# Optimization experiments

Hardware: AMD Instinct MI355X
Metric: run time of the kernel (lower is better)

The kernel has to match this reference:

```python
import jax, jax.numpy as jnp
import numpy as np

EPS = 1e-5
N_HEADS = 8
NEG = -1e32


def _pos_emb(S, D):
    # CosinePositionalEmbedding: sin/cos fully overwrite the random init for even D
    pos = jnp.arange(S, dtype=jnp.float32)[:, None]
    div = jnp.exp(jnp.arange(0, D, 2, dtype=jnp.float32) * (-np.log(10000.0) / D))
    pe = jnp.zeros((S, D), dtype=jnp.float32)
    pe = pe.at[:, 0::2].set(jnp.sin(pos * div))
    pe = pe.at[:, 1::2].set(jnp.cos(pos * div))
    return pe


def _ln(x, g, b):
    mu = jnp.mean(x, axis=-1, keepdims=True)
    var = jnp.mean((x - mu) ** 2, axis=-1, keepdims=True)
    return (x - mu) / jnp.sqrt(var + EPS) * g + b


def setup_inputs() -> dict:
    key = jax.random.key(0)
    B, S, D, FF, L = 32, 512, 512, 2048, 4
    ks = jax.random.split(key, 8)
    w = 0.02
    return {
        "q_embed_data": jax.random.normal(ks[0], (B, S, D), jnp.float32),
        "qa_embed_data": jax.random.normal(ks[1], (B, S, D), jnp.float32),
        "boost_focus": jax.random.uniform(ks[2], (1,), jnp.float32),
        "Wk": w * jax.random.normal(ks[3], (L, D, D), jnp.float32),
        "bk": jnp.zeros((L, D), jnp.float32),
        "Wv": w * jax.random.normal(ks[4], (L, D, D), jnp.float32),
        "bv": jnp.zeros((L, D), jnp.float32),
        "Wo": w * jax.random.normal(ks[5], (L, D, D), jnp.float32),
        "bo": jnp.zeros((L, D), jnp.float32),
        "ln1_g": jnp.ones((L, D), jnp.float32),
        "ln1_b": jnp.zeros((L, D), jnp.float32),
        "W1": w * jax.random.normal(ks[6], (L, D, FF), jnp.float32),
        "b1": jnp.zeros((L, FF), jnp.float32),
        "W2": w * jax.random.normal(ks[7], (L, FF, D), jnp.float32),
        "b2": jnp.zeros((L, D), jnp.float32),
        "ln2_g": jnp.ones((L, D), jnp.float32),
        "ln2_b": jnp.zeros((L, D), jnp.float32),
    }


def reference(q_embed_data, qa_embed_data, boost_focus, Wk, bk, Wv, bv, Wo, bo,
              ln1_g, ln1_b, W1, b1, W2, b2, ln2_g, ln2_b):
    B, S, D = q_embed_data.shape
    L = Wk.shape[0]
    H = N_HEADS
    dk = D // H
    bf = boost_focus[0]
    pe = _pos_emb(S, D)
    x = q_embed_data + pe[None]          # query/key stream
    y = qa_embed_data + pe[None]         # value stream (fixed across blocks)
    # mask=0: triu(k=0)==0 -> only strictly past positions (j < i) allowed
    allowed = jnp.tril(jnp.ones((S, S), bool), k=-1)
    scale = 1.0 / np.sqrt(dk)
    for l in range(L):
        # kq_same=True: q and k both use k_linear on x -> identical projections
        qk = (x @ Wk[l] + bk[l]).reshape(B, S, H, dk).transpose(0, 2, 1, 3)
        v = (y @ Wv[l] + bv[l]).reshape(B, S, H, dk).transpose(0, 2, 1, 3)
        scores = jnp.einsum('bhid,bhjd->bhij', qk, qk) * scale * (1.0 + bf)
        scores = jnp.where(allowed, scores, NEG)
        probs = jax.nn.softmax(scores, axis=-1)
        probs = probs.at[:, :, 0, :].set(0.0)  # zero_pad: first query row zeroed
        attn = jnp.einsum('bhij,bhjd->bhid', probs, v)
        attn = attn.transpose(0, 2, 1, 3).reshape(B, S, D) @ Wo[l] + bo[l]
        x = _ln(x + attn, ln1_g[l], ln1_b[l])
        ff = jax.nn.relu(x @ W1[l] + b1[l]) @ W2[l] + b2[l]
        x = _ln(x + ff, ln2_g[l], ln2_b[l])
    return x
```

## Files before the change

kernel.cpp:

```cpp
#include <hip/hip_runtime.h>
#include <hip/hip_bf16.h>

typedef __bf16 bf16_t;
typedef __bf16 bf16x4 __attribute__((ext_vector_type(4)));
typedef __bf16 bf16x8 __attribute__((ext_vector_type(8)));
typedef float f32x4 __attribute__((ext_vector_type(4)));

union FragU { bf16x8 v; bf16x4 h[2]; };
union F4U { float4 v; float f[4]; };

constexpr int BB = 32, SS = 512, DD = 512, FFD = 2048, LL = 4, HH = 8;

__device__ __forceinline__ int permk(int k) {
  int g = (k >> 2) & 7;
  int pos = (g < 4) ? (g << 1) : (((g - 4) << 1) | 1);
  return (k & ~31) | (pos << 2) | (k & 3);
}

__device__ __forceinline__ void gload_lds16(const bf16_t* g, bf16_t* l) {
  __builtin_amdgcn_global_load_lds(
      (const __attribute__((address_space(1))) void*)g,
      (__attribute__((address_space(3))) void*)l, 16, 0, 0);
}

template<int N> __device__ __forceinline__ void vmwait() {
  asm volatile("s_waitcnt vmcnt(%0)" :: "n"(N) : "memory");
}
__device__ __forceinline__ void barrier_raw() {
  asm volatile("s_barrier" ::: "memory");
}

__global__ void pe_kernel(float* __restrict__ pe) {
  int idx = blockIdx.x * blockDim.x + threadIdx.x;
  if (idx >= SS * DD / 2) return;
  int p = idx % (DD / 2);
  int s = idx / (DD / 2);
  float div = expf((float)(2 * p) * (-9.210340371976184f / (float)DD));
  float a = (float)s * div;
  pe[s * DD + 2 * p]     = sinf(a);
  pe[s * DD + 2 * p + 1] = cosf(a);
}

__global__ __launch_bounds__(256) void tcast_kernel(const float* __restrict__ src,
                                                    bf16_t* __restrict__ dst,
                                                    int K, int N) {
  __shared__ float tile[32][33];
  size_t mat = (size_t)blockIdx.z * (size_t)K * (size_t)N;
  int k0 = blockIdx.y * 32, n0 = blockIdx.x * 32;
  int t = threadIdx.x;
  int r = t >> 3, c4 = (t & 7) * 4;
  const float4 v = *reinterpret_cast<const float4*>(&src[mat + (size_t)(k0 + r) * N + n0 + c4]);
  tile[r][c4 + 0] = v.x; tile[r][c4 + 1] = v.y; tile[r][c4 + 2] = v.z; tile[r][c4 + 3] = v.w;
  __syncthreads();
  bf16x4 o;
  o[0] = (bf16_t)tile[c4 + 0][r];
  o[1] = (bf16_t)tile[c4 + 1][r];
  o[2] = (bf16_t)tile[c4 + 2][r];
  o[3] = (bf16_t)tile[c4 + 3][r];
  *reinterpret_cast<bf16x4*>(&dst[mat + permk((n0 + r) * K + k0 + c4)]) = o;
}

__global__ void addpe_kernel(const float* __restrict__ q, const float* __restrict__ qa,
                             const float* __restrict__ pe,
                             float* __restrict__ x, bf16_t* __restrict__ xb,
                             bf16_t* __restrict__ yb) {
  int i = blockIdx.x * blockDim.x + threadIdx.x;
  int pei = i & (SS * DD / 4 - 1);
  float4 pv = reinterpret_cast<const float4*>(pe)[pei];
  float4 qv = reinterpret_cast<const float4*>(q)[i];
  float4 av = reinterpret_cast<const float4*>(qa)[i];
  float4 xv = make_float4(qv.x + pv.x, qv.y + pv.y, qv.z + pv.z, qv.w + pv.w);
  float4 yv = make_float4(av.x + pv.x, av.y + pv.y, av.z + pv.z, av.w + pv.w);
  reinterpret_cast<float4*>(x)[i] = xv;
  bf16x4 xo, yo;
  xo[0] = (bf16_t)xv.x; xo[1] = (bf16_t)xv.y; xo[2] = (bf16_t)xv.z; xo[3] = (bf16_t)xv.w;
  yo[0] = (bf16_t)yv.x; yo[1] = (bf16_t)yv.y; yo[2] = (bf16_t)yv.z; yo[3] = (bf16_t)yv.w;
  int kp = permk(4 * i);
  *reinterpret_cast<bf16x4*>(&xb[kp]) = xo;
  *reinterpret_cast<bf16x4*>(&yb[kp]) = yo;
}

template<int OMODE, bool RELU>
__global__ __launch_bounds__(256, 2) void gemm_kernel(const bf16_t* __restrict__ A,
                                                      const bf16_t* __restrict__ Bt,
                                                      const float* __restrict__ bias,
                                                      void* __restrict__ Cout,
                                                      int N, int K, int nnt) {
  __shared__ bf16_t a_s[2][128 * 64];
  __shared__ bf16_t b_s[2][128 * 64];
  const int t = threadIdx.x;
  const int nwg = gridDim.x;
  const int bid = blockIdx.x;
  const int wg = (bid & 7) * (nwg >> 3) + (bid >> 3);
  const int m0 = (wg / nnt) * 128, n0 = (wg % nnt) * 128;
  const int l = t & 63, w = t >> 6, g = l >> 4, ln = l & 15;
  const int wm = (w >> 1) * 64, wn = (w & 1) * 64;
  const int tr = t >> 3;
  const int bsrc = ((t & 7) ^ (tr & 7)) * 8;
  const bf16_t* Asrc = A + (size_t)(m0 + tr) * K + bsrc;
  const bf16_t* Bsrc = Bt + (size_t)(n0 + tr) * K + bsrc;
  const size_t rstr = (size_t)32 * K;
  const int x0 = (g ^ (ln & 7)) * 8;
  const int x1 = ((4 + g) ^ (ln & 7)) * 8;

  auto STAGE = [&](int p, int T) {
    const int k0 = T << 6;
#pragma unroll
    for (int i = 0; i < 4; i++) gload_lds16(Asrc + k0 + i * rstr, &a_s[p][(i * 256 + t) * 8]);
#pragma unroll
    for (int i = 0; i < 4; i++) gload_lds16(Bsrc + k0 + i * rstr, &b_s[p][(i * 256 + t) * 8]);
  };

  f32x4 acc[4][4] = {};
  const int NT = K >> 6;
  STAGE(0, 0);
  STAGE(1, 1);
  for (int T = 0; T < NT; T++) {
    const int p = T & 1;
    if (T + 1 < NT) vmwait<8>(); else vmwait<0>();
    barrier_raw();
    __builtin_amdgcn_sched_barrier(0);
#pragma unroll
    for (int kc = 0; kc < 2; kc++) {
      const int xo = kc ? x1 : x0;
      FragU fa[4], fb[4];
#pragma unroll
      for (int mi = 0; mi < 4; mi++)
        fa[mi].v = *reinterpret_cast<const bf16x8*>(&a_s[p][(wm + mi * 16 + ln) * 64 + xo]);
#pragma unroll
      for (int ni = 0; ni < 4; ni++)
        fb[ni].v = *reinterpret_cast<const bf16x8*>(&b_s[p][(wn + ni * 16 + ln) * 64 + xo]);
      __builtin_amdgcn_s_setprio(1);
#pragma unroll
      for (int mi = 0; mi < 4; mi++)
#pragma unroll
        for (int ni = 0; ni < 4; ni++)
          acc[mi][ni] = __builtin_amdgcn_mfma_f32_16x16x32_bf16(fa[mi].v, fb[ni].v, acc[mi][ni], 0, 0, 0);
      __builtin_amdgcn_s_setprio(0);
    }
    __builtin_amdgcn_sched_barrier(0);
    barrier_raw();
    if (T + 2 < NT) STAGE(p, T + 2);
  }

  if constexpr (OMODE == 2) {
    const int brow = m0 >> 9;
    const int s0b = (m0 & 511) + wm;
    bf16_t* vout = reinterpret_cast<bf16_t*>(Cout);
#pragma unroll
    for (int ni = 0; ni < 4; ni++) {
      const int d = n0 + wn + ni * 16 + ln;
      const float bv = bias[d];
      const int h = d >> 6, dd = d & 63;
      bf16_t* vrow = vout + ((size_t)((brow * HH + h) * 64 + dd)) * SS;
#pragma unroll
      for (int mi = 0; mi < 4; mi++) {
        const int s0 = s0b + mi * 16 + g * 4;
        const int jt = s0 >> 6, jj = s0 & 63;
        const int js = jj >> 5, half = (jj >> 4) & 1;
        const int blkx = (js * 4 + g) ^ (dd & 7);
        bf16x4 o;
#pragma unroll
        for (int r = 0; r < 4; r++) o[r] = (bf16_t)(acc[mi][ni][r] + bv);
        *reinterpret_cast<bf16x4*>(&vrow[jt * 64 + blkx * 8 + half * 4]) = o;
      }
    }
  } else {
#pragma unroll
    for (int ni = 0; ni < 4; ni++) {
      const int col = n0 + wn + ni * 16 + ln;
      const float bv = bias[col];
      const int colp = (OMODE == 1) ? permk(col) : col;
#pragma unroll
      for (int mi = 0; mi < 4; mi++)
#pragma unroll
        for (int r = 0; r < 4; r++) {
          int row = m0 + wm + mi * 16 + g * 4 + r;
          float o = acc[mi][ni][r] + bv;
          if (RELU) o = fmaxf(o, 0.f);
          if (OMODE == 1)
            reinterpret_cast<bf16_t*>(Cout)[(size_t)row * N + colp] = (bf16_t)o;
          else
            reinterpret_cast<float*>(Cout)[(size_t)row * N + col] = o;
        }
    }
  }
}

__global__ __launch_bounds__(256) void ln_kernel(const float* __restrict__ xin,
                                                 const float* __restrict__ addv,
                                                 const float* __restrict__ gamma,
                                                 const float* __restrict__ beta,
                                                 float* __restrict__ xout,
                                                 bf16_t* __restrict__ xbout) {
  int row = blockIdx.x * 4 + (threadIdx.x >> 6);
  int l = threadIdx.x & 63;
  const float* px = xin + (size_t)row * DD;
  const float* pa = addv + (size_t)row * DD;
  float vals[8];
  float s = 0.f;
#pragma unroll
  for (int i = 0; i < 2; i++) {
    float4 a = reinterpret_cast<const float4*>(px)[l * 2 + i];
    float4 b = reinterpret_cast<const float4*>(pa)[l * 2 + i];
    vals[i * 4 + 0] = a.x + b.x;
    vals[i * 4 + 1] = a.y + b.y;
    vals[i * 4 + 2] = a.z + b.z;
    vals[i * 4 + 3] = a.w + b.w;
  }
#pragma unroll
  for (int j = 0; j < 8; j++) s += vals[j];
#pragma unroll
  for (int off = 1; off < 64; off <<= 1) s += __shfl_xor(s, off, 64);
  float mean = s * (1.f / DD);
  float sq = 0.f;
#pragma unroll
  for (int j = 0; j < 8; j++) { float d = vals[j] - mean; sq += d * d; }
#pragma unroll
  for (int off = 1; off < 64; off <<= 1) sq += __shfl_xor(sq, off, 64);
  float rstd = rsqrtf(sq * (1.f / DD) + 1e-5f);
#pragma unroll
  for (int i = 0; i < 2; i++) {
    F4U o; bf16x4 ob;
#pragma unroll
    for (int j = 0; j < 4; j++) {
      int colj = l * 8 + i * 4 + j;
      float v = (vals[i * 4 + j] - mean) * rstd * gamma[colj] + beta[colj];
      o.f[j] = v;
      ob[j] = (bf16_t)v;
    }
    reinterpret_cast<float4*>(xout + (size_t)row * DD)[l * 2 + i] = o.v;
    *reinterpret_cast<bf16x4*>(&xbout[(size_t)row * DD + permk(l * 8 + i * 4)]) = ob;
  }
}

__global__ __launch_bounds__(256) void attn_kernel(const bf16_t* __restrict__ qk,
                                                   const bf16_t* __restrict__ vtg,
                                                   bf16_t* __restrict__ outp,
                                                   const float* __restrict__ bfp) {
  __shared__ bf16_t k_s[64 * 64];
  __shared__ bf16_t v_t[64 * 64];
  const int bx = blockIdx.x, h = blockIdx.y, b = blockIdx.z;
  const int t = threadIdx.x, l = t & 63, w = t >> 6, g = l >> 4, ln = l & 15;
  const float sc = 0.125f * (1.f + bfp[0]);
  const size_t base = ((size_t)b * SS) * DD + h * 64;
  const bf16_t* vbase = vtg + ((size_t)((b * HH + h) * 64)) * SS;
  const int NQT = SS / 64;

  for (int pass = 0; pass < 2; pass++) {
    const int qt = pass ? (NQT - 1 - bx) : bx;
    const int i0 = qt * 64;
    FragU qB[2];
    {
      const bf16_t* qp = qk + base + (size_t)(i0 + w * 16 + ln) * DD;
      qB[0].v = *reinterpret_cast<const bf16x8*>(&qp[g * 8]);
      qB[1].v = *reinterpret_cast<const bf16x8*>(&qp[32 + g * 8]);
    }
    float m = -1e30f, lrow = 0.f;
    f32x4 acc[4] = {};
    const int iql = w * 16 + ln;

    for (int kt = 0; kt <= qt; kt++) {
      const int j0 = kt * 64;
      __syncthreads();
      {
        int c1 = t + 256;
        int jr0 = t >> 3, bb0 = t & 7;
        int jr1 = c1 >> 3, bb1 = c1 & 7;
        gload_lds16(qk + base + (size_t)(j0 + jr0) * DD + ((bb0 ^ (jr0 & 7)) * 8), &k_s[t * 8]);
        gload_lds16(qk + base + (size_t)(j0 + jr1) * DD + ((bb1 ^ (jr1 & 7)) * 8), &k_s[c1 * 8]);
        gload_lds16(vbase + (size_t)jr0 * SS + j0 + bb0 * 8, &v_t[t * 8]);
        gload_lds16(vbase + (size_t)jr1 * SS + j0 + bb1 * 8, &v_t[c1 * 8]);
      }
      asm volatile("s_waitcnt vmcnt(0)" ::: "memory");
      __syncthreads();
      f32x4 sfr[4] = {};
#pragma unroll
      for (int ks = 0; ks < 2; ks++)
#pragma unroll
        for (int nj = 0; nj < 4; nj++) {
          int jc = nj * 16 + ln;
          FragU ka;
          ka.v = *reinterpret_cast<const bf16x8*>(&k_s[jc * 64 + (((ks * 4 + g) ^ (jc & 7)) * 8)]);
          sfr[nj] = __builtin_amdgcn_mfma_f32_16x16x32_bf16(ka.v, qB[ks].v, sfr[nj], 0, 0, 0);
        }
      if (kt == qt) {
#pragma unroll
        for (int nj = 0; nj < 4; nj++)
#pragma unroll
          for (int r = 0; r < 4; r++)
            if (nj * 16 + g * 4 + r >= iql) sfr[nj][r] = -1e30f;
      }
      float pm = -1e30f;
#pragma unroll
      for (int nj = 0; nj < 4; nj++)
#pragma unroll
        for (int r = 0; r < 4; r++) pm = fmaxf(pm, sfr[nj][r]);
      pm = fmaxf(pm, __shfl_xor(pm, 16, 64));
      pm = fmaxf(pm, __shfl_xor(pm, 32, 64));
      float mnew = fmaxf(m, pm);
      float fac = __expf(sc * (m - mnew));
      m = mnew;
      float ps = 0.f;
#pragma unroll
      for (int nj = 0; nj < 4; nj++)
#pragma unroll
        for (int r = 0; r < 4; r++) {
          float p = __expf(sc * (sfr[nj][r] - m));
          sfr[nj][r] = p;
          ps += p;
        }
      ps += __shfl_xor(ps, 16, 64);
      ps += __shfl_xor(ps, 32, 64);
      lrow = lrow * fac + ps;
      float facr[4];
#pragma unroll
      for (int r = 0; r < 4; r++) facr[r] = __shfl(fac, g * 4 + r, 64);
#pragma unroll
      for (int nd = 0; nd < 4; nd++)
#pragma unroll
        for (int r = 0; r < 4; r++) acc[nd][r] *= facr[r];
      FragU pa[2];
#pragma unroll
      for (int js = 0; js < 2; js++)
#pragma unroll
        for (int kk = 0; kk < 4; kk++) {
          pa[js].v[kk]     = (bf16_t)sfr[js * 2][kk];
          pa[js].v[kk + 4] = (bf16_t)sfr[js * 2 + 1][kk];
        }
#pragma unroll
      for (int js = 0; js < 2; js++)
#pragma unroll
        for (int nd = 0; nd < 4; nd++) {
          int d = nd * 16 + ln;
          FragU vb;
          vb.v = *reinterpret_cast<const bf16x8*>(&v_t[d * 64 + (((js * 4 + g) ^ (d & 7)) * 8)]);
          acc[nd] = __builtin_amdgcn_mfma_f32_16x16x32_bf16(pa[js].v, vb.v, acc[nd], 0, 0, 0);
        }
    }
    float lr[4];
#pragma unroll
    for (int r = 0; r < 4; r++) lr[r] = __shfl(lrow, g * 4 + r, 64);
    const int orow0 = i0 + w * 16 + g * 4;
#pragma unroll
    for (int nd = 0; nd < 4; nd++) {
      const int colp = permk(nd * 16 + ln);
#pragma unroll
      for (int r = 0; r < 4; r++) {
        int grow = orow0 + r;
        float o = (grow > 0 && lr[r] > 0.f) ? acc[nd][r] / lr[r] : 0.f;
        outp[base + (size_t)grow * DD + colp] = (bf16_t)o;
      }
    }
  }
}

extern "C" void kernel_launch(void* const* d_in, const int* in_sizes, int n_in,
                              void* d_out, int out_size, void* d_ws, size_t ws_size,
                              hipStream_t stream) {
  const float* q_emb  = (const float*)d_in[0];
  const float* qa_emb = (const float*)d_in[1];
  const float* bfp    = (const float*)d_in[2];
  const float* Wk  = (const float*)d_in[3];
  const float* bk  = (const float*)d_in[4];
  const float* Wv  = (const float*)d_in[5];
  const float* bv  = (const float*)d_in[6];
  const float* Wo  = (const float*)d_in[7];
  const float* bo  = (const float*)d_in[8];
  const float* g1  = (const float*)d_in[9];
  const float* be1 = (const float*)d_in[10];
  const float* W1  = (const float*)d_in[11];
  const float* b1  = (const float*)d_in[12];
  const float* W2  = (const float*)d_in[13];
  const float* b2  = (const float*)d_in[14];
  const float* g2  = (const float*)d_in[15];
  const float* be2 = (const float*)d_in[16];
  float* out = (float*)d_out;
  (void)in_sizes; (void)n_in; (void)out_size; (void)ws_size;

  char* wsp = (char*)d_ws;
  size_t off = 0;
  auto alloc = [&](size_t bytes) -> void* {
    void* p = wsp + off;
    off += (bytes + 255) & ~(size_t)255;
    return p;
  };
  const size_t BSD = (size_t)BB * SS * DD;
  float*  pe   = (float*) alloc((size_t)SS * DD * 4);
  float*  x    = (float*) alloc(BSD * 4);
  float*  tmp  = (float*) alloc(BSD * 4);
  bf16_t* xb   = (bf16_t*)alloc(BSD * 2);
  bf16_t* yb   = (bf16_t*)alloc(BSD * 2);
  bf16_t* qkb  = (bf16_t*)alloc(BSD * 2);
  bf16_t* vtg  = (bf16_t*)alloc(BSD * 2);
  bf16_t* atb  = (bf16_t*)alloc(BSD * 2);
  bf16_t* h1   = (bf16_t*)alloc((size_t)BB * SS * FFD * 2);
  bf16_t* Wkb  = (bf16_t*)alloc((size_t)LL * DD * DD * 2);
  bf16_t* Wvb  = (bf16_t*)alloc((size_t)LL * DD * DD * 2);
  bf16_t* Wob  = (bf16_t*)alloc((size_t)LL * DD * DD * 2);
  bf16_t* W1b  = (bf16_t*)alloc((size_t)LL * DD * FFD * 2);
  bf16_t* W2b  = (bf16_t*)alloc((size_t)LL * FFD * DD * 2);

  pe_kernel<<<(SS * DD / 2 + 255) / 256, 256, 0, stream>>>(pe);
  tcast_kernel<<<dim3(DD / 32, DD / 32, LL), 256, 0, stream>>>(Wk, Wkb, DD, DD);
  tcast_kernel<<<dim3(DD / 32, DD / 32, LL), 256, 0, stream>>>(Wv, Wvb, DD, DD);
  tcast_kernel<<<dim3(DD / 32, DD / 32, LL), 256, 0, stream>>>(Wo, Wob, DD, DD);
  tcast_kernel<<<dim3(FFD / 32, DD / 32, LL), 256, 0, stream>>>(W1, W1b, DD, FFD);
  tcast_kernel<<<dim3(DD / 32, FFD / 32, LL), 256, 0, stream>>>(W2, W2b, FFD, DD);
  addpe_kernel<<<(int)(BSD / 4 / 256), 256, 0, stream>>>(q_emb, qa_emb, pe, x, xb, yb);

  const int M = BB * SS;
  const int nD = (M / 128) * (DD / 128);
  const int nF = (M / 128) * (FFD / 128);
  dim3 gA(SS / 128, HH, BB);
  for (int layer = 0; layer < LL; layer++) {
    const bf16_t* Wkl = Wkb + (size_t)layer * DD * DD;
    const bf16_t* Wvl = Wvb + (size_t)layer * DD * DD;
    const bf16_t* Wol = Wob + (size_t)layer * DD * DD;
    const bf16_t* W1l = W1b + (size_t)layer * DD * FFD;
    const bf16_t* W2l = W2b + (size_t)layer * FFD * DD;
    gemm_kernel<1, false><<<nD, 256, 0, stream>>>(xb, Wkl, bk + layer * DD, qkb, DD, DD, DD / 128);
    gemm_kernel<2, false><<<nD, 256, 0, stream>>>(yb, Wvl, bv + layer * DD, vtg, DD, DD, DD / 128);
    attn_kernel<<<gA, 256, 0, stream>>>(qkb, vtg, atb, bfp);
    gemm_kernel<0, false><<<nD, 256, 0, stream>>>(atb, Wol, bo + layer * DD, tmp, DD, DD, DD / 128);
    ln_kernel<<<M / 4, 256, 0, stream>>>(x, tmp, g1 + layer * DD, be1 + layer * DD, x, xb);
    gemm_kernel<1, true><<<nF, 256, 0, stream>>>(xb, W1l, b1 + layer * FFD, h1, FFD, DD, FFD / 128);
    gemm_kernel<0, false><<<nD, 256, 0, stream>>>(h1, W2l, b2 + layer * DD, tmp, DD, FFD, DD / 128);
    float* xo = (layer == LL - 1) ? out : x;
    ln_kernel<<<M / 4, 256, 0, stream>>>(x, tmp, g2 + layer * DD, be2 + layer * DD, xo, xb);
  }
}
```

Baseline: 828.5 us.

## Replace GEMM with 256x128 tile, triple-buffered LDS pipeline and staged epilogue

```diff
diff --git a/kernel.cpp b/kernel.cpp
--- a/kernel.cpp
+++ b/kernel.cpp
@@ -16,6 +16,11 @@
   int pos = (g < 4) ? (g << 1) : (((g - 4) << 1) | 1);
   return (k & ~31) | (pos << 2) | (k & 3);
 }
+__device__ __forceinline__ int permpos(int c) {
+  int gq = c >> 2;
+  int pos = (gq < 4) ? (gq << 1) : (((gq - 4) << 1) | 1);
+  return pos * 4 + (c & 3);
+}
 
 __device__ __forceinline__ void gload_lds16(const bf16_t* g, bf16_t* l) {
   __builtin_amdgcn_global_load_lds(
@@ -25,6 +30,9 @@
 
 template<int N> __device__ __forceinline__ void vmwait() {
   asm volatile("s_waitcnt vmcnt(%0)" :: "n"(N) : "memory");
+}
+__device__ __forceinline__ void lgkmwait0() {
+  asm volatile("s_waitcnt lgkmcnt(0)" ::: "memory");
 }
 __device__ __forceinline__ void barrier_raw() {
   asm volatile("s_barrier" ::: "memory");
@@ -81,108 +89,184 @@
 }
 
 template<int OMODE, bool RELU>
-__global__ __launch_bounds__(256, 2) void gemm_kernel(const bf16_t* __restrict__ A,
-                                                      const bf16_t* __restrict__ Bt,
-                                                      const float* __restrict__ bias,
-                                                      void* __restrict__ Cout,
-                                                      int N, int K, int nnt) {
-  __shared__ bf16_t a_s[2][128 * 64];
-  __shared__ bf16_t b_s[2][128 * 64];
+__global__ __launch_bounds__(512, 1) void gemm3_kernel(const bf16_t* __restrict__ A,
+                                                       const bf16_t* __restrict__ Bt,
+                                                       const float* __restrict__ bias,
+                                                       void* __restrict__ Cout,
+                                                       int N, int K, int nnt) {
+  constexpr int BM = 256, BN = 128;
+  __shared__ bf16_t a_s[3][BM * 64];
+  __shared__ bf16_t b_s[3][BN * 64];
   const int t = threadIdx.x;
-  const int nwg = gridDim.x;
-  const int bid = blockIdx.x;
+  const int bid = blockIdx.x, nwg = gridDim.x;
   const int wg = (bid & 7) * (nwg >> 3) + (bid >> 3);
-  const int m0 = (wg / nnt) * 128, n0 = (wg % nnt) * 128;
+  const int m0 = (wg / nnt) * BM, n0 = (wg % nnt) * BN;
   const int l = t & 63, w = t >> 6, g = l >> 4, ln = l & 15;
-  const int wm = (w >> 1) * 64, wn = (w & 1) * 64;
+  const int wr = w >> 1, wc = w & 1;
   const int tr = t >> 3;
   const int bsrc = ((t & 7) ^ (tr & 7)) * 8;
   const bf16_t* Asrc = A + (size_t)(m0 + tr) * K + bsrc;
   const bf16_t* Bsrc = Bt + (size_t)(n0 + tr) * K + bsrc;
-  const size_t rstr = (size_t)32 * K;
+  const size_t rstr = (size_t)64 * K;
   const int x0 = (g ^ (ln & 7)) * 8;
   const int x1 = ((4 + g) ^ (ln & 7)) * 8;
 
-  auto STAGE = [&](int p, int T) {
+  auto ST0 = [&](int q, int T) {
     const int k0 = T << 6;
-#pragma unroll
-    for (int i = 0; i < 4; i++) gload_lds16(Asrc + k0 + i * rstr, &a_s[p][(i * 256 + t) * 8]);
-#pragma unroll
-    for (int i = 0; i < 4; i++) gload_lds16(Bsrc + k0 + i * rstr, &b_s[p][(i * 256 + t) * 8]);
+    gload_lds16(Asrc + k0,        &a_s[q][(0 * 512 + t) * 8]);
+    gload_lds16(Asrc + k0 + rstr, &a_s[q][(1 * 512 + t) * 8]);
+    gload_lds16(Bsrc + k0,        &b_s[q][(0 * 512 + t) * 8]);
+  };
+  auto ST1 = [&](int q, int T) {
+    const int k0 = T << 6;
+    gload_lds16(Asrc + k0 + 2 * rstr, &a_s[q][(2 * 512 + t) * 8]);
+    gload_lds16(Asrc + k0 + 3 * rstr, &a_s[q][(3 * 512 + t) * 8]);
+    gload_lds16(Bsrc + k0 + rstr,     &b_s[q][(1 * 512 + t) * 8]);
   };
 
   f32x4 acc[4][4] = {};
   const int NT = K >> 6;
-  STAGE(0, 0);
-  STAGE(1, 1);
+  ST0(0, 0); ST1(0, 0);
+  ST0(1, 1); ST1(1, 1);
+  vmwait<6>();
+  barrier_raw();
+
+  int q = 0;
   for (int T = 0; T < NT; T++) {
-    const int p = T & 1;
-    if (T + 1 < NT) vmwait<8>(); else vmwait<0>();
-    barrier_raw();
-    __builtin_amdgcn_sched_barrier(0);
-#pragma unroll
-    for (int kc = 0; kc < 2; kc++) {
-      const int xo = kc ? x1 : x0;
+    const int q2 = (q + 2 >= 3) ? (q - 1) : (q + 2);
+    const bool st = (T + 2) < NT;
+    {
       FragU fa[4], fb[4];
 #pragma unroll
       for (int mi = 0; mi < 4; mi++)
-        fa[mi].v = *reinterpret_cast<const bf16x8*>(&a_s[p][(wm + mi * 16 + ln) * 64 + xo]);
-#pragma unroll
-      for (int ni = 0; ni < 4; ni++)
-        fb[ni].v = *reinterpret_cast<const bf16x8*>(&b_s[p][(wn + ni * 16 + ln) * 64 + xo]);
+        fa[mi].v = *reinterpret_cast<const bf16x8*>(&a_s[q][(wr * 64 + mi * 16 + ln) * 64 + x0]);
+#pragma unroll
+      for (int nf = 0; nf < 4; nf++)
+        fb[nf].v = *reinterpret_cast<const bf16x8*>(&b_s[q][(wc * 64 + nf * 16 + ln) * 64 + x0]);
+      if (st) ST0(q2, T + 2);
+      barrier_raw();
+      lgkmwait0();
+      __builtin_amdgcn_sched_barrier(0);
       __builtin_amdgcn_s_setprio(1);
 #pragma unroll
       for (int mi = 0; mi < 4; mi++)
 #pragma unroll
-        for (int ni = 0; ni < 4; ni++)
-          acc[mi][ni] = __builtin_amdgcn_mfma_f32_16x16x32_bf16(fa[mi].v, fb[ni].v, acc[mi][ni], 0, 0, 0);
+        for (int nf = 0; nf < 4; nf++)
+          acc[mi][nf] = __builtin_amdgcn_mfma_f32_16x16x32_bf16(fa[mi].v, fb[nf].v, acc[mi][nf], 0, 0, 0);
       __builtin_amdgcn_s_setprio(0);
-    }
-    __builtin_amdgcn_sched_barrier(0);
-    barrier_raw();
-    if (T + 2 < NT) STAGE(p, T + 2);
+      barrier_raw();
+    }
+    {
+      FragU fa[4], fb[4];
+#pragma unroll
+      for (int mi = 0; mi < 4; mi++)
+        fa[mi].v = *reinterpret_cast<const bf16x8*>(&a_s[q][(wr * 64 + mi * 16 + ln) * 64 + x1]);
+#pragma unroll
+      for (int nf = 0; nf < 4; nf++)
+        fb[nf].v = *reinterpret_cast<const bf16x8*>(&b_s[q][(wc * 64 + nf * 16 + ln) * 64 + x1]);
+      if (st) ST1(q2, T + 2);
+      barrier_raw();
+      lgkmwait0();
+      __builtin_amdgcn_sched_barrier(0);
+      __builtin_amdgcn_s_setprio(1);
+#pragma unroll
+      for (int mi = 0; mi < 4; mi++)
+#pragma unroll
+        for (int nf = 0; nf < 4; nf++)
+          acc[mi][nf] = __builtin_amdgcn_mfma_f32_16x16x32_bf16(fa[mi].v, fb[nf].v, acc[mi][nf], 0, 0, 0);
+      __builtin_amdgcn_s_setprio(0);
+      if (T + 1 < NT) { if (st) vmwait<6>(); else vmwait<0>(); }
+      barrier_raw();
+    }
+    q = (q + 1 == 3) ? 0 : q + 1;
   }
 
-  if constexpr (OMODE == 2) {
+  if constexpr (OMODE == 1) {
+    bf16_t* eps = &a_s[0][0];
+#pragma unroll
+    for (int nf = 0; nf < 4; nf++) {
+      const int col_l = wc * 64 + nf * 16 + ln;
+      const float bv = bias[n0 + col_l];
+      const int colp = (col_l & ~31) | permpos(col_l & 31);
+#pragma unroll
+      for (int mi = 0; mi < 4; mi++)
+#pragma unroll
+        for (int r = 0; r < 4; r++) {
+          int row = wr * 64 + mi * 16 + g * 4 + r;
+          float o = acc[mi][nf][r] + bv;
+          if (RELU) o = fmaxf(o, 0.f);
+          eps[row * 136 + colp] = (bf16_t)o;
+        }
+    }
+    __syncthreads();
+    bf16_t* outp = reinterpret_cast<bf16_t*>(Cout);
+#pragma unroll
+    for (int rd = 0; rd < 8; rd++) {
+      int idx = rd * 512 + t;
+      int row = idx >> 4, c = idx & 15;
+      bf16x8 v = *reinterpret_cast<const bf16x8*>(&eps[row * 136 + c * 8]);
+      *reinterpret_cast<bf16x8*>(&outp[(size_t)(m0 + row) * N + n0 + c * 8]) = v;
+    }
+  } else if constexpr (OMODE == 0) {
+    float* epf = reinterpret_cast<float*>(&a_s[0][0]);
+    float* outp = reinterpret_cast<float*>(Cout);
+    for (int hh = 0; hh < 2; hh++) {
+      __syncthreads();
+      if ((wr >> 1) == hh) {
+        const int rb = (wr & 1) * 64;
+#pragma unroll
+        for (int nf = 0; nf < 4; nf++) {
+          const int col_l = wc * 64 + nf * 16 + ln;
+          const float bv = bias[n0 + col_l];
+#pragma unroll
+          for (int mi = 0; mi < 4; mi++)
+#pragma unroll
+            for (int r = 0; r < 4; r++) {
+              int row = rb + mi * 16 + g * 4 + r;
+              epf[row * 132 + col_l] = acc[mi][nf][r] + bv;
+            }
+        }
+      }
+      __syncthreads();
+#pragma unroll
+      for (int rd = 0; rd < 8; rd++) {
+        int idx = rd * 512 + t;
+        int row = idx >> 5, c = idx & 31;
+        float4 v = *reinterpret_cast<const float4*>(&epf[row * 132 + c * 4]);
+        *reinterpret_cast<float4*>(&outp[(size_t)(m0 + hh * 128 + row) * N + n0 + c * 4]) = v;
+      }
+    }
+  } else {
+    bf16_t* epv = &a_s[0][0];
+#pragma unroll
+    for (int nf = 0; nf < 4; nf++) {
+      const int d_l = wc * 64 + nf * 16 + ln;
+      const int d = n0 + d_l;
+      const float bv = bias[d];
+      const int dd = d & 63;
+#pragma unroll
+      for (int mi = 0; mi < 4; mi++) {
+        int s0 = wr * 64 + mi * 16 + g * 4;
+        int jt_l = s0 >> 6, jj = s0 & 63;
+        int js = jj >> 5, half = (jj >> 4) & 1;
+        int blkx = (js * 4 + g) ^ (dd & 7);
+        bf16x4 o;
+#pragma unroll
+        for (int r = 0; r < 4; r++) o[r] = (bf16_t)(acc[mi][nf][r] + bv);
+        *reinterpret_cast<bf16x4*>(&epv[d_l * 264 + jt_l * 64 + blkx * 8 + half * 4]) = o;
+      }
+    }
+    __syncthreads();
+    bf16_t* vout = reinterpret_cast<bf16_t*>(Cout);
     const int brow = m0 >> 9;
-    const int s0b = (m0 & 511) + wm;
-    bf16_t* vout = reinterpret_cast<bf16_t*>(Cout);
-#pragma unroll
-    for (int ni = 0; ni < 4; ni++) {
-      const int d = n0 + wn + ni * 16 + ln;
-      const float bv = bias[d];
-      const int h = d >> 6, dd = d & 63;
-      bf16_t* vrow = vout + ((size_t)((brow * HH + h) * 64 + dd)) * SS;
-#pragma unroll
-      for (int mi = 0; mi < 4; mi++) {
-        const int s0 = s0b + mi * 16 + g * 4;
-        const int jt = s0 >> 6, jj = s0 & 63;
-        const int js = jj >> 5, half = (jj >> 4) & 1;
-        const int blkx = (js * 4 + g) ^ (dd & 7);
-        bf16x4 o;
-#pragma unroll
-        for (int r = 0; r < 4; r++) o[r] = (bf16_t)(acc[mi][ni][r] + bv);
-        *reinterpret_cast<bf16x4*>(&vrow[jt * 64 + blkx * 8 + half * 4]) = o;
-      }
-    }
-  } else {
-#pragma unroll
-    for (int ni = 0; ni < 4; ni++) {
-      const int col = n0 + wn + ni * 16 + ln;
-      const float bv = bias[col];
-      const int colp = (OMODE == 1) ? permk(col) : col;
-#pragma unroll
-      for (int mi = 0; mi < 4; mi++)
-#pragma unroll
-        for (int r = 0; r < 4; r++) {
-          int row = m0 + wm + mi * 16 + g * 4 + r;
-          float o = acc[mi][ni][r] + bv;
-          if (RELU) o = fmaxf(o, 0.f);
-          if (OMODE == 1)
-            reinterpret_cast<bf16_t*>(Cout)[(size_t)row * N + colp] = (bf16_t)o;
-          else
-            reinterpret_cast<float*>(Cout)[(size_t)row * N + col] = o;
-        }
+#pragma unroll
+    for (int rd = 0; rd < 8; rd++) {
+      int idx = rd * 512 + t;
+      int d_l = idx >> 5, c = idx & 31;
+      bf16x8 v = *reinterpret_cast<const bf16x8*>(&epv[d_l * 264 + c * 8]);
+      int d = n0 + d_l, h = d >> 6, dd = d & 63;
+      *reinterpret_cast<bf16x8*>(
+          &vout[((size_t)((brow * HH + h) * 64 + dd)) * SS + (m0 & 511) + c * 8]) = v;
     }
   }
 }
@@ -410,8 +494,8 @@
   addpe_kernel<<<(int)(BSD / 4 / 256), 256, 0, stream>>>(q_emb, qa_emb, pe, x, xb, yb);
 
   const int M = BB * SS;
-  const int nD = (M / 128) * (DD / 128);
-  const int nF = (M / 128) * (FFD / 128);
+  const int nD3 = (M / 256) * (DD / 128);
+  const int nF3 = (M / 256) * (FFD / 128);
   dim3 gA(SS / 128, HH, BB);
   for (int layer = 0; layer < LL; layer++) {
     const bf16_t* Wkl = Wkb + (size_t)layer * DD * DD;
@@ -419,13 +503,13 @@
     const bf16_t* Wol = Wob + (size_t)layer * DD * DD;
     const bf16_t* W1l = W1b + (size_t)layer * DD * FFD;
     const bf16_t* W2l = W2b + (size_t)layer * FFD * DD;
-    gemm_kernel<1, false><<<nD, 256, 0, stream>>>(xb, Wkl, bk + layer * DD, qkb, DD, DD, DD / 128);
-    gemm_kernel<2, false><<<nD, 256, 0, stream>>>(yb, Wvl, bv + layer * DD, vtg, DD, DD, DD / 128);
+    gemm3_kernel<1, false><<<nD3, 512, 0, stream>>>(xb, Wkl, bk + layer * DD, qkb, DD, DD, DD / 128);
+    gemm3_kernel<2, false><<<nD3, 512, 0, stream>>>(yb, Wvl, bv + layer * DD, vtg, DD, DD, DD / 128);
     attn_kernel<<<gA, 256, 0, stream>>>(qkb, vtg, atb, bfp);
-    gemm_kernel<0, false><<<nD, 256, 0, stream>>>(atb, Wol, bo + layer * DD, tmp, DD, DD, DD / 128);
+    gemm3_kernel<0, false><<<nD3, 512, 0, stream>>>(atb, Wol, bo + layer * DD, tmp, DD, DD, DD / 128);
     ln_kernel<<<M / 4, 256, 0, stream>>>(x, tmp, g1 + layer * DD, be1 + layer * DD, x, xb);
-    gemm_kernel<1, true><<<nF, 256, 0, stream>>>(xb, W1l, b1 + layer * FFD, h1, FFD, DD, FFD / 128);
-    gemm_kernel<0, false><<<nD, 256, 0, stream>>>(h1, W2l, b2 + layer * DD, tmp, DD, FFD, DD / 128);
+    gemm3_kernel<1, true><<<nF3, 512, 0, stream>>>(xb, W1l, b1 + layer * FFD, h1, FFD, DD, FFD / 128);
+    gemm3_kernel<0, false><<<nD3, 512, 0, stream>>>(h1, W2l, b2 + layer * DD, tmp, DD, FFD, DD / 128);
     float* xo = (layer == LL - 1) ? out : x;
     ln_kernel<<<M / 4, 256, 0, stream>>>(x, tmp, g2 + layer * DD, be2 + layer * DD, xo, xb);
   }
```

New measurement: 883.4 us. 1.07x slower.

## Add 256x256 eight-wave GEMM for FFN up-projection and double-buffer attention KV

Applied to the files above, without the earlier changes.

```diff
diff --git a/kernel.cpp b/kernel.cpp
--- a/kernel.cpp
+++ b/kernel.cpp
@@ -26,9 +26,14 @@
 template<int N> __device__ __forceinline__ void vmwait() {
   asm volatile("s_waitcnt vmcnt(%0)" :: "n"(N) : "memory");
 }
+__device__ __forceinline__ void lgkmwait0() {
+  asm volatile("s_waitcnt lgkmcnt(0)" ::: "memory");
+}
 __device__ __forceinline__ void barrier_raw() {
   asm volatile("s_barrier" ::: "memory");
 }
+
+#define MFMA_ACC(d, a, b) d = __builtin_amdgcn_mfma_f32_16x16x32_bf16((a).v, (b).v, d, 0, 0, 0)
 
 __global__ void pe_kernel(float* __restrict__ pe) {
   int idx = blockIdx.x * blockDim.x + threadIdx.x;
@@ -135,7 +140,7 @@
       for (int mi = 0; mi < 4; mi++)
 #pragma unroll
         for (int ni = 0; ni < 4; ni++)
-          acc[mi][ni] = __builtin_amdgcn_mfma_f32_16x16x32_bf16(fa[mi].v, fb[ni].v, acc[mi][ni], 0, 0, 0);
+          MFMA_ACC(acc[mi][ni], fa[mi], fb[ni]);
       __builtin_amdgcn_s_setprio(0);
     }
     __builtin_amdgcn_sched_barrier(0);
@@ -184,6 +189,126 @@
             reinterpret_cast<float*>(Cout)[(size_t)row * N + col] = o;
         }
     }
+  }
+}
+
+__global__ __launch_bounds__(512, 1) void gemmW_kernel(const bf16_t* __restrict__ A,
+                                                       const bf16_t* __restrict__ Bt,
+                                                       const float* __restrict__ bias,
+                                                       bf16_t* __restrict__ Cout,
+                                                       int N, int K, int nnt) {
+  __shared__ bf16_t a_s[2][256 * 64];
+  __shared__ bf16_t b_s[2][256 * 64];
+  const int t = threadIdx.x;
+  const int bid = blockIdx.x, nwg = gridDim.x;
+  const int wg = (bid & 7) * (nwg >> 3) + (bid >> 3);
+  const int m0 = (wg / nnt) * 256, n0 = (wg % nnt) * 256;
+  const int l = t & 63, w = t >> 6, g = l >> 4, ln = l & 15, lnx = l & 7;
+  const int wr = w >> 2, wc = w & 3;
+  const int tr = t >> 3;
+  const int bsrc = ((t & 7) ^ (tr & 7)) * 8;
+  const bf16_t* Asrc = A + (size_t)(m0 + tr) * K + bsrc;
+  const bf16_t* Bsrc = Bt + (size_t)(n0 + tr) * K + bsrc;
+  const size_t rstr = (size_t)64 * K;
+  const int x0 = (g ^ lnx) * 8;
+  const int x1 = ((4 + g) ^ lnx) * 8;
+
+  auto STA = [&](int q, int T2, int i) {
+    gload_lds16(Asrc + (T2 << 6) + i * rstr, &a_s[q][(i * 512 + t) * 8]);
+  };
+  auto STB = [&](int q, int T2, int i) {
+    gload_lds16(Bsrc + (T2 << 6) + i * rstr, &b_s[q][(i * 512 + t) * 8]);
+  };
+
+  f32x4 acc[8][4] = {};
+  const int NT = K >> 6;
+#pragma unroll
+  for (int i = 0; i < 4; i++) { STA(0, 0, i); STB(0, 0, i); }
+#pragma unroll
+  for (int i = 0; i < 4; i++) { STA(1, 1, i); STB(1, 1, i); }
+  vmwait<8>();
+  barrier_raw();
+
+  for (int T = 0; T < NT; T++) {
+    const int p = T & 1;
+    const bool st = (T + 2) < NT;
+    FragU fa[4], fb[4];
+#pragma unroll
+    for (int mf = 0; mf < 4; mf++)
+      fa[mf].v = *reinterpret_cast<const bf16x8*>(&a_s[p][(wr * 128 + mf * 16 + ln) * 64 + x0]);
+#pragma unroll
+    for (int nf = 0; nf < 4; nf++)
+      fb[nf].v = *reinterpret_cast<const bf16x8*>(&b_s[p][(wc * 64 + nf * 16 + ln) * 64 + x0]);
+    barrier_raw();
+    lgkmwait0();
+    __builtin_amdgcn_sched_barrier(0);
+    __builtin_amdgcn_s_setprio(1);
+#pragma unroll
+    for (int mf = 0; mf < 4; mf++)
+#pragma unroll
+      for (int nf = 0; nf < 4; nf++) MFMA_ACC(acc[mf][nf], fa[mf], fb[nf]);
+    __builtin_amdgcn_s_setprio(0);
+    barrier_raw();
+#pragma unroll
+    for (int mf = 0; mf < 4; mf++)
+      fa[mf].v = *reinterpret_cast<const bf16x8*>(&a_s[p][(wr * 128 + 64 + mf * 16 + ln) * 64 + x0]);
+    barrier_raw();
+    lgkmwait0();
+    __builtin_amdgcn_sched_barrier(0);
+    __builtin_amdgcn_s_setprio(1);
+#pragma unroll
+    for (int mf = 0; mf < 4; mf++)
+#pragma unroll
+      for (int nf = 0; nf < 4; nf++) MFMA_ACC(acc[4 + mf][nf], fa[mf], fb[nf]);
+    __builtin_amdgcn_s_setprio(0);
+    barrier_raw();
+#pragma unroll
+    for (int mf = 0; mf < 4; mf++)
+      fa[mf].v = *reinterpret_cast<const bf16x8*>(&a_s[p][(wr * 128 + mf * 16 + ln) * 64 + x1]);
+#pragma unroll
+    for (int nf = 0; nf < 4; nf++)
+      fb[nf].v = *reinterpret_cast<const bf16x8*>(&b_s[p][(wc * 64 + nf * 16 + ln) * 64 + x1]);
+    barrier_raw();
+    if (st) { STA(p, T + 2, 0); STA(p, T + 2, 2); STB(p, T + 2, 0); STB(p, T + 2, 1); STB(p, T + 2, 2); STB(p, T + 2, 3); }
+    lgkmwait0();
+    __builtin_amdgcn_sched_barrier(0);
+    __builtin_amdgcn_s_setprio(1);
+#pragma unroll
+    for (int mf = 0; mf < 4; mf++)
+#pragma unroll
+      for (int nf = 0; nf < 4; nf++) MFMA_ACC(acc[mf][nf], fa[mf], fb[nf]);
+    __builtin_amdgcn_s_setprio(0);
+    barrier_raw();
+#pragma unroll
+    for (int mf = 0; mf < 4; mf++)
+      fa[mf].v = *reinterpret_cast<const bf16x8*>(&a_s[p][(wr * 128 + 64 + mf * 16 + ln) * 64 + x1]);
+    barrier_raw();
+    if (st) { STA(p, T + 2, 1); STA(p, T + 2, 3); }
+    lgkmwait0();
+    __builtin_amdgcn_sched_barrier(0);
+    __builtin_amdgcn_s_setprio(1);
+#pragma unroll
+    for (int mf = 0; mf < 4; mf++)
+#pragma unroll
+      for (int nf = 0; nf < 4; nf++) MFMA_ACC(acc[4 + mf][nf], fa[mf], fb[nf]);
+    __builtin_amdgcn_s_setprio(0);
+    if (T + 1 < NT) { if (st) vmwait<8>(); else vmwait<0>(); }
+    barrier_raw();
+  }
+
+#pragma unroll
+  for (int nf = 0; nf < 4; nf++) {
+    const int col = n0 + wc * 64 + nf * 16 + ln;
+    const float bv = bias[col];
+    const int colp = permk(col);
+#pragma unroll
+    for (int mf = 0; mf < 8; mf++)
+#pragma unroll
+      for (int r = 0; r < 4; r++) {
+        int row = m0 + wr * 128 + mf * 16 + g * 4 + r;
+        float o = fmaxf(acc[mf][nf][r] + bv, 0.f);
+        Cout[(size_t)row * N + colp] = (bf16_t)o;
+      }
   }
 }
 
@@ -238,8 +363,8 @@
                                                    const bf16_t* __restrict__ vtg,
                                                    bf16_t* __restrict__ outp,
                                                    const float* __restrict__ bfp) {
-  __shared__ bf16_t k_s[64 * 64];
-  __shared__ bf16_t v_t[64 * 64];
+  __shared__ bf16_t k_s[2][64 * 64];
+  __shared__ bf16_t v_t[2][64 * 64];
   const int bx = blockIdx.x, h = blockIdx.y, b = blockIdx.z;
   const int t = threadIdx.x, l = t & 63, w = t >> 6, g = l >> 4, ln = l & 15;
   const float sc = 0.125f * (1.f + bfp[0]);
@@ -247,9 +372,20 @@
   const bf16_t* vbase = vtg + ((size_t)((b * HH + h) * 64)) * SS;
   const int NQT = SS / 64;
 
+  auto STAGEKV = [&](int q, int j0) {
+    int c1 = t + 256;
+    int jr0 = t >> 3, bb0 = t & 7;
+    int jr1 = c1 >> 3, bb1 = c1 & 7;
+    gload_lds16(qk + base + (size_t)(j0 + jr0) * DD + ((bb0 ^ (jr0 & 7)) * 8), &k_s[q][t * 8]);
+    gload_lds16(qk + base + (size_t)(j0 + jr1) * DD + ((bb1 ^ (jr1 & 7)) * 8), &k_s[q][c1 * 8]);
+    gload_lds16(vbase + (size_t)jr0 * SS + j0 + bb0 * 8, &v_t[q][t * 8]);
+    gload_lds16(vbase + (size_t)jr1 * SS + j0 + bb1 * 8, &v_t[q][c1 * 8]);
+  };
+
   for (int pass = 0; pass < 2; pass++) {
     const int qt = pass ? (NQT - 1 - bx) : bx;
     const int i0 = qt * 64;
+    STAGEKV(0, 0);
     FragU qB[2];
     {
       const bf16_t* qp = qk + base + (size_t)(i0 + w * 16 + ln) * DD;
@@ -262,18 +398,11 @@
 
     for (int kt = 0; kt <= qt; kt++) {
       const int j0 = kt * 64;
-      __syncthreads();
-      {
-        int c1 = t + 256;
-        int jr0 = t >> 3, bb0 = t & 7;
-        int jr1 = c1 >> 3, bb1 = c1 & 7;
-        gload_lds16(qk + base + (size_t)(j0 + jr0) * DD + ((bb0 ^ (jr0 & 7)) * 8), &k_s[t * 8]);
-        gload_lds16(qk + base + (size_t)(j0 + jr1) * DD + ((bb1 ^ (jr1 & 7)) * 8), &k_s[c1 * 8]);
-        gload_lds16(vbase + (size_t)jr0 * SS + j0 + bb0 * 8, &v_t[t * 8]);
-        gload_lds16(vbase + (size_t)jr1 * SS + j0 + bb1 * 8, &v_t[c1 * 8]);
-      }
-      asm volatile("s_waitcnt vmcnt(0)" ::: "memory");
-      __syncthreads();
+      const int p = kt & 1;
+      if (kt < qt) { STAGEKV(p ^ 1, j0 + 64); vmwait<4>(); }
+      else vmwait<0>();
+      barrier_raw();
+      __builtin_amdgcn_sched_barrier(0);
       f32x4 sfr[4] = {};
 #pragma unroll
       for (int ks = 0; ks < 2; ks++)
@@ -281,7 +410,7 @@
         for (int nj = 0; nj < 4; nj++) {
           int jc = nj * 16 + ln;
           FragU ka;
-          ka.v = *reinterpret_cast<const bf16x8*>(&k_s[jc * 64 + (((ks * 4 + g) ^ (jc & 7)) * 8)]);
+          ka.v = *reinterpret_cast<const bf16x8*>(&k_s[p][jc * 64 + (((ks * 4 + g) ^ (jc & 7)) * 8)]);
           sfr[nj] = __builtin_amdgcn_mfma_f32_16x16x32_bf16(ka.v, qB[ks].v, sfr[nj], 0, 0, 0);
         }
       if (kt == qt) {
@@ -306,9 +435,9 @@
       for (int nj = 0; nj < 4; nj++)
 #pragma unroll
         for (int r = 0; r < 4; r++) {
-          float p = __expf(sc * (sfr[nj][r] - m));
-          sfr[nj][r] = p;
-          ps += p;
+          float p2 = __expf(sc * (sfr[nj][r] - m));
+          sfr[nj][r] = p2;
+          ps += p2;
         }
       ps += __shfl_xor(ps, 16, 64);
       ps += __shfl_xor(ps, 32, 64);
@@ -334,9 +463,10 @@
         for (int nd = 0; nd < 4; nd++) {
           int d = nd * 16 + ln;
           FragU vb;
-          vb.v = *reinterpret_cast<const bf16x8*>(&v_t[d * 64 + (((js * 4 + g) ^ (d & 7)) * 8)]);
+          vb.v = *reinterpret_cast<const bf16x8*>(&v_t[p][d * 64 + (((js * 4 + g) ^ (d & 7)) * 8)]);
           acc[nd] = __builtin_amdgcn_mfma_f32_16x16x32_bf16(pa[js].v, vb.v, acc[nd], 0, 0, 0);
         }
+      barrier_raw();
     }
     float lr[4];
 #pragma unroll
@@ -411,7 +541,7 @@
 
   const int M = BB * SS;
   const int nD = (M / 128) * (DD / 128);
-  const int nF = (M / 128) * (FFD / 128);
+  const int nW = (M / 256) * (FFD / 256);
   dim3 gA(SS / 128, HH, BB);
   for (int layer = 0; layer < LL; layer++) {
     const bf16_t* Wkl = Wkb + (size_t)layer * DD * DD;
@@ -424,7 +554,7 @@
     attn_kernel<<<gA, 256, 0, stream>>>(qkb, vtg, atb, bfp);
     gemm_kernel<0, false><<<nD, 256, 0, stream>>>(atb, Wol, bo + layer * DD, tmp, DD, DD, DD / 128);
     ln_kernel<<<M / 4, 256, 0, stream>>>(x, tmp, g1 + layer * DD, be1 + layer * DD, x, xb);
-    gemm_kernel<1, true><<<nF, 256, 0, stream>>>(xb, W1l, b1 + layer * FFD, h1, FFD, DD, FFD / 128);
+    gemmW_kernel<<<nW, 512, 0, stream>>>(xb, W1l, b1 + layer * FFD, h1, FFD, DD, FFD / 256);
     gemm_kernel<0, false><<<nD, 256, 0, stream>>>(h1, W2l, b2 + layer * DD, tmp, DD, FFD, DD / 128);
     float* xo = (layer == LL - 1) ? out : x;
     ln_kernel<<<M / 4, 256, 0, stream>>>(x, tmp, g2 + layer * DD, be2 + layer * DD, xo, xb);
```

Result: slower. 887.3 us (+7.1%).
